# Kernel tuning notes

Hardware: AMD Instinct MI355X
Metric: run time of the kernel (lower is better)

The kernel has to match this reference:

```python
import jax, jax.numpy as jnp
import numpy as np

D_MODEL = 1024
N_HEADS = 16
D_HEAD = D_MODEL // N_HEADS
D_FF = 4096
BATCH = 2
SEQ = 2048
EPS = 1e-5


def setup_inputs() -> dict:
    key = jax.random.key(0)
    ks = jax.random.split(key, 8)
    s = 0.02
    x = jax.random.normal(ks[0], (BATCH, SEQ, D_MODEL), dtype=jnp.float32)
    # Per-head projection weights, stacked: [H, d_head, d_model] (torch Linear stores (out,in))
    wq = jax.random.normal(ks[1], (N_HEADS, D_HEAD, D_MODEL), dtype=jnp.float32) * s
    wk = jax.random.normal(ks[2], (N_HEADS, D_HEAD, D_MODEL), dtype=jnp.float32) * s
    wv = jax.random.normal(ks[3], (N_HEADS, D_HEAD, D_MODEL), dtype=jnp.float32) * s
    wo = jax.random.normal(ks[4], (D_MODEL, D_MODEL), dtype=jnp.float32) * s
    w1 = jax.random.normal(ks[5], (D_FF, D_MODEL), dtype=jnp.float32) * s
    w2 = jax.random.normal(ks[6], (D_MODEL, D_FF), dtype=jnp.float32) * s
    ln1_g = jnp.ones((D_MODEL,), jnp.float32)
    ln1_b = jnp.zeros((D_MODEL,), jnp.float32)
    ln2_g = jnp.ones((D_MODEL,), jnp.float32)
    ln2_b = jnp.zeros((D_MODEL,), jnp.float32)
    return {"x": x, "wq": wq, "wk": wk, "wv": wv, "wo": wo,
            "w1": w1, "w2": w2, "ln1_g": ln1_g, "ln1_b": ln1_b,
            "ln2_g": ln2_g, "ln2_b": ln2_b}


def _layer_norm(x, g, b):
    mu = jnp.mean(x, axis=-1, keepdims=True)
    var = jnp.mean(jnp.square(x - mu), axis=-1, keepdims=True)
    return (x - mu) * jax.lax.rsqrt(var + EPS) * g + b


def _mha(h, wq, wk, wv, wo):
    # h: [b,s,d]; wq/wk/wv: [H,dh,d] -> q/k/v: [b,H,s,dh]
    q = jnp.einsum('bsd,hed->bhse', h, wq)
    k = jnp.einsum('bsd,hed->bhse', h, wk)
    v = jnp.einsum('bsd,hed->bhse', h, wv)
    scores = jnp.einsum('bhqe,bhke->bhqk', q, k) / jnp.sqrt(jnp.float32(D_HEAD))
    weights = jax.nn.softmax(scores, axis=-1)
    ctx = jnp.einsum('bhqk,bhke->bhqe', weights, v)  # [b,H,s,dh]
    # concat heads in order (head 0 first) -> [b,s,H*dh]
    concat = jnp.transpose(ctx, (0, 2, 1, 3)).reshape(h.shape[0], h.shape[1], D_MODEL)
    return concat @ wo.T


def reference(x, wq, wk, wv, wo, w1, w2, ln1_g, ln1_b, ln2_g, ln2_b):
    h = _layer_norm(x, ln1_g, ln1_b)
    attn_out = _mha(h, wq, wk, wv, wo)
    h2 = _layer_norm(x + attn_out, ln2_g, ln2_b)
    ff = jax.nn.gelu(h2 @ w1.T, approximate=False) @ w2.T
    return x + ff
```

## Files before the change

kernel.cpp:

```cpp
#include <hip/hip_runtime.h>
#include <hip/hip_bf16.h>
#include <math.h>

typedef __bf16 bf16_t;
typedef __bf16 bf16x8 __attribute__((ext_vector_type(8)));
typedef __bf16 bf16x4 __attribute__((ext_vector_type(4)));
typedef float f32x4 __attribute__((ext_vector_type(4)));
typedef unsigned int u32;
typedef u32 u32x2 __attribute__((ext_vector_type(2)));

#define DM 1024
#define SEQL 2048
#define NTOK 4096
#define QKVN 3072

__device__ __forceinline__ void gload_lds16(const bf16_t* g, bf16_t* l){
  __builtin_amdgcn_global_load_lds((const __attribute__((address_space(1))) void*)g,
                                   (__attribute__((address_space(3))) void*)l, 16, 0, 0);
}
__device__ __forceinline__ u32 ldsoff(const void* p){
  return (u32)(size_t)(__attribute__((address_space(3))) const void*)p;
}
__device__ __forceinline__ u32x2 tr64(u32 byte_off){
  u32x2 d;
  asm volatile("ds_read_b64_tr_b16 %0, %1" : "=v"(d) : "v"(byte_off));
  return d;
}
__device__ __forceinline__ u32 pack2(float a, float b){
  union{ __bf16 h[2]; u32 w; } z;
  z.h[0]=(__bf16)a; z.h[1]=(__bf16)b; return z.w;
}
__device__ __forceinline__ float gelu_fast(float x){
  const float y = 0.79788456f*(x + 0.044715f*x*x*x);
  float a = y*2.885390082f;
  a = fminf(fmaxf(a, -30.f), 30.f);
  const float t = __builtin_amdgcn_exp2f(a);
  const float th = (t-1.0f)*__builtin_amdgcn_rcpf(t+1.0f);
  return 0.5f*x*(1.0f+th);
}

__global__ __launch_bounds__(256) void prep_kernel(
    const float* __restrict__ wq, const float* __restrict__ wk,
    const float* __restrict__ wv, const float* __restrict__ wo,
    const float* __restrict__ w1, const float* __restrict__ w2,
    const float* __restrict__ x,  const float* __restrict__ g1,
    const float* __restrict__ b1,
    bf16_t* __restrict__ wqkv_b, bf16_t* __restrict__ wo_b,
    bf16_t* __restrict__ w1_b,   bf16_t* __restrict__ w2_b,
    bf16_t* __restrict__ h1)
{
  __shared__ float red[8];
  const int bid = blockIdx.x;
  const int t = threadIdx.x;
  if (bid < 12288){
    const int flat = (bid*256 + t)*4;
    const int seg = flat >> 20;
    const int off1m = flat & 1048575;
    const float* src; bf16_t* dst;
    if (seg < 3){
      src = (seg==0 ? wq : (seg==1 ? wk : wv)) + off1m;
      dst = wqkv_b + flat;
    } else if (seg == 3){
      src = wo + off1m;  dst = wo_b + off1m;
    } else if (seg < 8){
      src = w1 + (flat - 4*1048576);  dst = w1_b + (flat - 4*1048576);
    } else {
      src = w2 + (flat - 8*1048576);  dst = w2_b + (flat - 8*1048576);
    }
    const float4 v = *(const float4*)src;
    bf16x4 o; o[0]=(__bf16)v.x; o[1]=(__bf16)v.y; o[2]=(__bf16)v.z; o[3]=(__bf16)v.w;
    *(bf16x4*)dst = o;
  } else {
    const int row = bid - 12288;
    const float4 v = *(const float4*)(x + (size_t)row*DM + t*4);
    float s  = v.x+v.y+v.z+v.w;
    float sq = v.x*v.x+v.y*v.y+v.z*v.z+v.w*v.w;
    #pragma unroll
    for (int m=1;m<64;m<<=1){ s += __shfl_xor(s,m); sq += __shfl_xor(sq,m); }
    const int w = t>>6;
    if ((t&63)==0){ red[w]=s; red[4+w]=sq; }
    __syncthreads();
    s  = red[0]+red[1]+red[2]+red[3];
    sq = red[4]+red[5]+red[6]+red[7];
    const float mean = s*(1.f/DM);
    const float var  = sq*(1.f/DM) - mean*mean;
    const float rstd = rsqrtf(var + 1e-5f);
    const float4 gg = *(const float4*)(g1 + t*4);
    const float4 bb = *(const float4*)(b1 + t*4);
    bf16x4 o;
    o[0]=(__bf16)((v.x-mean)*rstd*gg.x+bb.x);
    o[1]=(__bf16)((v.y-mean)*rstd*gg.y+bb.y);
    o[2]=(__bf16)((v.z-mean)*rstd*gg.z+bb.z);
    o[3]=(__bf16)((v.w-mean)*rstd*gg.w+bb.w);
    *(bf16x4*)(h1 + (size_t)row*DM + t*4) = o;
  }
}

__global__ __launch_bounds__(256) void lnb_kernel(const bf16_t* __restrict__ in,
    const float* __restrict__ g, const float* __restrict__ bta,
    bf16_t* __restrict__ outp)
{
  const int row = blockIdx.x;
  const int t = threadIdx.x;
  const bf16x4 raw = *(const bf16x4*)(in + (size_t)row*DM + t*4);
  float4 v;
  v.x=(float)raw[0]; v.y=(float)raw[1]; v.z=(float)raw[2]; v.w=(float)raw[3];
  float s  = v.x+v.y+v.z+v.w;
  float sq = v.x*v.x+v.y*v.y+v.z*v.z+v.w*v.w;
  #pragma unroll
  for (int m=1;m<64;m<<=1){ s += __shfl_xor(s,m); sq += __shfl_xor(sq,m); }
  __shared__ float red[8];
  const int w = t>>6;
  if ((t&63)==0){ red[w]=s; red[4+w]=sq; }
  __syncthreads();
  s  = red[0]+red[1]+red[2]+red[3];
  sq = red[4]+red[5]+red[6]+red[7];
  const float mean = s*(1.f/DM);
  const float var  = sq*(1.f/DM) - mean*mean;
  const float rstd = rsqrtf(var + 1e-5f);
  const float4 gg = *(const float4*)(g + t*4);
  const float4 bb = *(const float4*)(bta + t*4);
  bf16x4 o;
  o[0]=(__bf16)((v.x-mean)*rstd*gg.x+bb.x);
  o[1]=(__bf16)((v.y-mean)*rstd*gg.y+bb.y);
  o[2]=(__bf16)((v.z-mean)*rstd*gg.z+bb.z);
  o[3]=(__bf16)((v.w-mean)*rstd*gg.w+bb.w);
  *(bf16x4*)(outp + (size_t)row*DM + t*4) = o;
}

__global__ __launch_bounds__(256) void red4_kernel(
    const bf16_t* __restrict__ p0, const bf16_t* __restrict__ p1,
    const bf16_t* __restrict__ p2, const bf16_t* __restrict__ p3,
    const float* __restrict__ x, float* __restrict__ outp)
{
  const int i = (blockIdx.x*256 + threadIdx.x)*4;
  const bf16x4 a0 = *(const bf16x4*)(p0 + i);
  const bf16x4 a1 = *(const bf16x4*)(p1 + i);
  const bf16x4 a2 = *(const bf16x4*)(p2 + i);
  const bf16x4 a3 = *(const bf16x4*)(p3 + i);
  const float4 xs = *(const float4*)(x + i);
  float4 o;
  o.x = xs.x + ((float)a0[0]+(float)a1[0]) + ((float)a2[0]+(float)a3[0]);
  o.y = xs.y + ((float)a0[1]+(float)a1[1]) + ((float)a2[1]+(float)a3[1]);
  o.z = xs.z + ((float)a0[2]+(float)a1[2]) + ((float)a2[2]+(float)a3[2]);
  o.w = xs.w + ((float)a0[3]+(float)a1[3]) + ((float)a2[3]+(float)a3[3]);
  *(float4*)(outp + i) = o;
}

template<int EPI>
__global__ __launch_bounds__(512, 2) void gemm8ph(
    const bf16_t* __restrict__ A, const bf16_t* __restrict__ Bw,
    void* __restrict__ c0, void* __restrict__ c1,
    void* __restrict__ c2, void* __restrict__ c3,
    int N, int K, int lda)
{
  __shared__ __align__(16) char ldsb[131072];
  const int tid = threadIdx.x, lane = tid&63, wid = tid>>6;
  const int q16 = lane&15, g = lane>>4;
  const int wm = wid>>2, wn = wid&3;

  const int flat = blockIdx.y*gridDim.x + blockIdx.x;
  const int xcd = flat&7, jj = flat>>3;
  const int NY = gridDim.y;
  const int jdiv = jj/NY, jmod = jj - jdiv*NY;
  const int bm = (xcd*2 + jdiv)*256, bn = jmod*256;
  const int sk = blockIdx.z;
  const int koff = sk*K;
  void* Cout = (sk==0) ? c0 : (sk==1) ? c1 : (sk==2) ? c2 : c3;

  int mloc, kloc;
  {
    const u32 L = tid*16;
    const u32 logical = L ^ (((L>>9)&1)<<5);
    mloc = (int)(logical>>6);
    kloc = (int)((logical&63)>>1);
  }
  const bf16_t* asrc = A  + (size_t)(bm + mloc)*lda + koff + kloc;
  const bf16_t* bsrc = Bw + (size_t)(bn + mloc)*lda + koff + kloc;
  const u32 laneOff = ((u32)(q16*64 + g*16)) ^ ((u32)(q16&8)<<2);

  f32x4 acc[8][4] = {};
  bf16x8 bv[4];

  auto stage = [&](int buf, int kh, int isB, int s){
    const bf16_t* src = isB ? bsrc : asrc;
    #pragma unroll
    for (int h2=0; h2<2; h2++)
      gload_lds16(src + (size_t)(h2*128)*lda + s*64 + kh*32,
                  (bf16_t*)(ldsb + buf*65536 + isB*32768 + kh*16384 + h2*8192 + tid*16));
  };

  stage(0,0,0,0); stage(0,0,1,0); stage(0,1,0,0); stage(0,1,1,0);
  stage(1,0,0,1); stage(1,0,1,1);
  asm volatile("s_waitcnt vmcnt(4)" ::: "memory");
  __builtin_amdgcn_s_barrier();

  const int NSTEP = K>>6;
  const int NIT = NSTEP>>1;

#define PHASE(BUF,KH,MH,DOST,SBUF,SKH,SISB,SSTEP,CK) { \
    bf16x8 av[4]; \
    const char* Ab_ = ldsb + (BUF)*65536 + (KH)*16384 + wm*8192; \
    _Pragma("unroll") for (int jx=0;jx<4;jx++) \
      av[jx] = *(const bf16x8*)(Ab_ + (((MH)*4+jx)<<10) + laneOff); \
    if ((MH)==0){ \
      const char* Bb_ = ldsb + (BUF)*65536 + 32768 + (KH)*16384 + (wn>>1)*8192; \
      _Pragma("unroll") for (int jx=0;jx<4;jx++) \
        bv[jx] = *(const bf16x8*)(Bb_ + ((((wn&1)*4)+jx)<<10) + laneOff); \
    } \
    if (DOST) stage(SBUF,SKH,SISB,SSTEP); \
    asm volatile("s_barrier" ::: "memory"); \
    asm volatile("s_waitcnt lgkmcnt(0)" ::: "memory"); \
    __builtin_amdgcn_s_setprio(1); \
    _Pragma("unroll") for (int jx=0;jx<4;jx++) \
      _Pragma("unroll") for (int j2=0;j2<4;j2++) \
        acc[(MH)*4+jx][j2] = __builtin_amdgcn_mfma_f32_16x16x32_bf16(av[jx], bv[j2], acc[(MH)*4+jx][j2],0,0,0); \
    __builtin_amdgcn_s_setprio(0); \
    if (CK){ if (nl) { asm volatile("s_waitcnt vmcnt(4)" ::: "memory"); } \
             else    { asm volatile("s_waitcnt vmcnt(0)" ::: "memory"); } } \
    asm volatile("s_barrier" ::: "memory"); }

  for (int it=0; it<NIT; it++){
    const int s0 = 2*it, s1 = s0+1;
    const bool nl = (it+1 < NIT);
    PHASE(0,0,0, 1,  1,1,0, s1,   0)
    PHASE(0,0,1, 1,  1,1,1, s1,   0)
    PHASE(0,1,0, nl, 0,0,0, s0+2, 0)
    PHASE(0,1,1, nl, 0,0,1, s0+2, 1)
    PHASE(1,0,0, nl, 0,1,0, s0+2, 0)
    PHASE(1,0,1, nl, 0,1,1, s0+2, 0)
    PHASE(1,1,0, nl, 1,0,0, s1+2, 0)
    PHASE(1,1,1, nl, 1,0,1, s1+2, 1)
  }
#undef PHASE

  #pragma unroll
  for (int fm=0; fm<8; fm++)
    #pragma unroll
    for (int fn=0; fn<4; fn++)
      #pragma unroll
      for (int i=0; i<4; i++){
        const int r = bm + wm*128 + fm*16 + g*4 + i;
        const int c = bn + wn*64 + fn*16 + q16;
        const size_t idx = (size_t)r*N + c;
        const float vv = acc[fm][fn][i];
        if constexpr (EPI==0){
          ((bf16_t*)Cout)[idx] = (__bf16)vv;
        } else {
          ((bf16_t*)Cout)[idx] = (__bf16)gelu_fast(vv);
        }
      }
}

template<int EPI>
__global__ __launch_bounds__(512, 2) void gemm128(
    const bf16_t* __restrict__ A, const bf16_t* __restrict__ Bw,
    void* __restrict__ Cout, const float* __restrict__ X,
    int N, int K)
{
  constexpr int BK = 32;
  __shared__ __align__(16) char ldsb[3*16384];
  const int tid = threadIdx.x, lane = tid&63, wid = tid>>6;
  const int q16 = lane&15, g = lane>>4;
  const int wm = wid>>2, wn = wid&3;

  const int flat = blockIdx.y*gridDim.x + blockIdx.x;
  const int xcd = flat&7, j = flat>>3;
  const int bm = ((xcd<<2) + (j>>3))*128, bn = (j&7)*128;

  int mloc, kloc;
  {
    const u32 L = tid*16;
    const u32 logical = L ^ (((L>>9)&1)<<5);
    mloc = (int)(logical>>6);
    kloc = (int)((logical&63)>>1);
  }
  const bf16_t* asrc = A  + (size_t)(bm + mloc)*K + kloc;
  const bf16_t* bsrc = Bw + (size_t)(bn + mloc)*K + kloc;
  const u32 laneOff = ((u32)(q16*64 + g*16)) ^ ((u32)(q16&8)<<2);

  f32x4 acc[4][2] = {};

  auto stageA = [&](int buf, int k0){
    gload_lds16(asrc + k0, (bf16_t*)(ldsb + buf*16384 + tid*16));
  };
  auto stageB = [&](int buf, int k0){
    gload_lds16(bsrc + k0, (bf16_t*)(ldsb + buf*16384 + 8192 + tid*16));
  };

  stageA(0,0); stageB(0,0);
  stageA(1,BK); stageB(1,BK);
  asm volatile("s_waitcnt vmcnt(2)" ::: "memory");
  __builtin_amdgcn_s_barrier();

  const int NT = K/BK;
  int bcur = 0;
  for (int kt=0; kt<NT; kt++){
    const int bstg = (bcur >= 1) ? bcur-1 : bcur+2;
    const char* Ab = ldsb + bcur*16384 + wm*4096;
    const char* Bb = ldsb + bcur*16384 + 8192 + wn*2048;
    const bool sOK = (kt+2 < NT);
    const int k0s = (kt+2)*BK;
    bf16x8 bv[2];
    #pragma unroll
    for (int p=0; p<2; p++){
      bf16x8 av[2];
      #pragma unroll
      for (int jx=0;jx<2;jx++)
        av[jx] = *(const bf16x8*)(Ab + ((p*2+jx)<<10) + laneOff);
      if (p==0){
        #pragma unroll
        for (int jx=0;jx<2;jx++)
          bv[jx] = *(const bf16x8*)(Bb + (jx<<10) + laneOff);
      }
      if (sOK){
        if (p==0) stageA(bstg,k0s);
        else      stageB(bstg,k0s);
      }
      asm volatile("s_barrier" ::: "memory");
      __builtin_amdgcn_s_setprio(1);
      #pragma unroll
      for (int jx=0;jx<2;jx++)
        #pragma unroll
        for (int j2=0;j2<2;j2++)
          acc[p*2+jx][j2] = __builtin_amdgcn_mfma_f32_16x16x32_bf16(av[jx], bv[j2], acc[p*2+jx][j2], 0,0,0);
      __builtin_amdgcn_s_setprio(0);
      if (p==1){
        if (sOK) asm volatile("s_waitcnt vmcnt(2)" ::: "memory");
        else     asm volatile("s_waitcnt vmcnt(0)" ::: "memory");
      }
      asm volatile("s_barrier" ::: "memory");
    }
    bcur = (bcur==2)?0:bcur+1;
  }

  #pragma unroll
  for (int fm=0; fm<4; fm++)
    #pragma unroll
    for (int fn=0; fn<2; fn++)
      #pragma unroll
      for (int i=0; i<4; i++){
        const int r = bm + wm*64 + fm*16 + g*4 + i;
        const int c = bn + wn*32 + fn*16 + q16;
        const size_t idx = (size_t)r*N + c;
        const float vv = X[idx] + acc[fm][fn][i];
        ((bf16_t*)Cout)[idx] = (__bf16)vv;
      }
}

__global__ __launch_bounds__(512, 4) void attn_kernel(
    const bf16_t* __restrict__ QKV, bf16_t* __restrict__ Ctx)
{
  __shared__ __align__(16) bf16_t Ks[2][128*64];
  __shared__ __align__(16) bf16_t Vs[2][32*4*72];
  const int tid = threadIdx.x, lane = tid&63, w = tid>>6;
  const int g = lane>>4, q16 = lane&15;
  const int bh = blockIdx.y, b = bh>>4, h = bh&15;
  const int qr0 = blockIdx.x*128 + w*16;
  const size_t tok0 = (size_t)b*SEQL;
  const int ch0 = h*64;

  bf16x8 aq[2];
  #pragma unroll
  for (int ks=0; ks<2; ks++){
    bf16x8 t = *(const bf16x8*)(QKV + (tok0+qr0+q16)*QKVN + ch0 + ks*32 + g*8);
    #pragma unroll
    for (int jx=0;jx<8;jx++) t[jx] = (__bf16)((float)t[jx]*0.18033688f);
    aq[ks] = t;
  }

  const int srow = tid>>3, sc8 = (tid&7)*8;
  const bf16_t* kptr_swz = QKV + (tok0+srow)*QKVN + 1024 + ch0 + (sc8 ^ ((srow&7)<<3));
  const bf16_t* vptr = QKV + (tok0+srow)*QKVN + 2048 + ch0 + sc8;
  const int vwoff = ((srow>>2)*4 + (sc8>>4))*72 + (srow&3)*16 + (sc8&15);

  float mrun = -1e30f, lrun = 0.f;
  f32x4 o[4] = {};

  #pragma unroll
  for (int it=0; it<2; it++)
    gload_lds16(kptr_swz + (size_t)(it*64)*QKVN, &Ks[0][tid*8 + it*4096]);
  bf16x8 vreg[2];
  #pragma unroll
  for (int it=0; it<2; it++)
    vreg[it] = *(const bf16x8*)(vptr + (size_t)(it*64)*QKVN);
  #pragma unroll
  for (int it=0; it<2; it++)
    *(bf16x8*)&Vs[0][vwoff + it*4608] = vreg[it];
  #pragma unroll
  for (int it=0; it<2; it++)
    vreg[it] = *(const bf16x8*)(vptr + (size_t)(128 + it*64)*QKVN);

  const int NT = SEQL/128;
  for (int t=0; t<NT; t++){
    __syncthreads();
    if (t+1 < NT){
      #pragma unroll
      for (int it=0; it<2; it++){
        gload_lds16(kptr_swz + (size_t)((t+1)*128 + it*64)*QKVN, &Ks[(t+1)&1][tid*8 + it*4096]);
        *(bf16x8*)&Vs[(t+1)&1][vwoff + it*4608] = vreg[it];
      }
      if (t+2 < NT){
        #pragma unroll
        for (int it=0; it<2; it++)
          vreg[it] = *(const bf16x8*)(vptr + (size_t)((t+2)*128 + it*64)*QKVN);
      }
    }
    const bf16_t* ksb = Ks[t&1];
    const u32 vs0 = ldsoff(&Vs[t&1][0]);

    f32x4 s[8] = {};
    #pragma unroll
    for (int ks=0; ks<2; ks++){
      #pragma unroll
      for (int fn=0; fn<8; fn++){
        const int r = fn*16 + q16;
        const int ce = ks*32 + g*8;
        bf16x8 bk = *(const bf16x8*)&ksb[r*64 + (ce ^ ((r&7)<<3))];
        s[fn] = __builtin_amdgcn_mfma_f32_16x16x32_bf16(bk, aq[ks], s[fn], 0, 0, 0);
      }
    }

    float mx = -1e30f;
    #pragma unroll
    for (int fn=0; fn<8; fn++)
      mx = fmaxf(mx, fmaxf(fmaxf(s[fn][0],s[fn][1]), fmaxf(s[fn][2],s[fn][3])));
    mx = fmaxf(mx, __shfl_xor(mx,16));
    mx = fmaxf(mx, __shfl_xor(mx,32));

    if (!__all(mx <= mrun + 11.54f)){
      const float mnew = fmaxf(mrun, mx);
      const float alpha = __builtin_amdgcn_exp2f(mrun - mnew);
      #pragma unroll
      for (int i=0;i<4;i++){
        const float ai = __shfl(alpha, g*4+i);
        o[0][i]*=ai; o[1][i]*=ai; o[2][i]*=ai; o[3][i]*=ai;
      }
      lrun *= alpha;
      mrun = mnew;
    }

    float rs = 0.f;
    u32 u[8][2];
    #pragma unroll
    for (int fn=0; fn<8; fn++){
      const float e0=__builtin_amdgcn_exp2f(s[fn][0]-mrun);
      const float e1=__builtin_amdgcn_exp2f(s[fn][1]-mrun);
      const float e2=__builtin_amdgcn_exp2f(s[fn][2]-mrun);
      const float e3=__builtin_amdgcn_exp2f(s[fn][3]-mrun);
      rs += (e0+e1)+(e2+e3);
      u[fn][0] = pack2(e0,e1);
      u[fn][1] = pack2(e2,e3);
    }
    rs += __shfl_xor(rs,16);
    rs += __shfl_xor(rs,32);
    lrun += rs;

    {
      u32x2 loA[4], hiA[4], loB[4], hiB[4];
      #pragma unroll
      for (int ne=0; ne<4; ne++){
        const u32 vb = vs0 + (u32)(((2*g*4 + ne)*72 + q16)*2);
        loA[ne] = tr64(vb);
        hiA[ne] = tr64(vb + 576);
      }
      #pragma unroll
      for (int ks=0; ks<4; ks++){
        union { u32 wd[4]; bf16x8 v; } pa;
        #pragma unroll
        for (int jj=0; jj<4; jj++){
          const int src = q16 + ((((g&1)<<1) + (jj>>1))<<4);
          const u32 a0 = (u32)__shfl((int)u[2*ks  ][jj&1], src);
          const u32 a1 = (u32)__shfl((int)u[2*ks+1][jj&1], src);
          pa.wd[jj] = (g&2) ? a1 : a0;
        }
        if (ks < 3){
          u32x2* nl_ = (ks&1) ? loA : loB;
          u32x2* nh_ = (ks&1) ? hiA : hiB;
          #pragma unroll
          for (int ne=0; ne<4; ne++){
            const u32 vb = vs0 + (u32)(((((ks+1)*8 + 2*g)*4 + ne)*72 + q16)*2);
            nl_[ne] = tr64(vb);
            nh_[ne] = tr64(vb + 576);
          }
          asm volatile("s_waitcnt lgkmcnt(8)" ::: "memory");
        } else {
          asm volatile("s_waitcnt lgkmcnt(0)" ::: "memory");
        }
        __builtin_amdgcn_sched_barrier(0);
        const u32x2* lo = (ks&1) ? loB : loA;
        const u32x2* hi = (ks&1) ? hiB : hiA;
        union { u32x2 u2[2]; bf16x8 v; } cc;
        #pragma unroll
        for (int ne=0; ne<4; ne++){
          cc.u2[0]=lo[ne]; cc.u2[1]=hi[ne];
          o[ne] = __builtin_amdgcn_mfma_f32_16x16x32_bf16(pa.v, cc.v, o[ne], 0, 0, 0);
        }
      }
    }
  }

  const float rl = 1.0f/lrun;
  #pragma unroll
  for (int i=0; i<4; i++){
    const float ri = __shfl(rl, g*4+i);
    #pragma unroll
    for (int ne=0; ne<4; ne++){
      const int r = qr0 + g*4 + i;
      Ctx[(tok0+r)*DM + ch0 + ne*16 + q16] = (__bf16)(o[ne][i]*ri);
    }
  }
}

extern "C" void kernel_launch(void* const* d_in, const int* in_sizes, int n_in,
                              void* d_out, int out_size, void* d_ws, size_t ws_size,
                              hipStream_t stream)
{
  (void)in_sizes; (void)n_in; (void)out_size; (void)ws_size;
  const float* x  = (const float*)d_in[0];
  const float* wq = (const float*)d_in[1];
  const float* wk = (const float*)d_in[2];
  const float* wv = (const float*)d_in[3];
  const float* wo = (const float*)d_in[4];
  const float* w1 = (const float*)d_in[5];
  const float* w2 = (const float*)d_in[6];
  const float* g1 = (const float*)d_in[7];
  const float* b1 = (const float*)d_in[8];
  const float* g2 = (const float*)d_in[9];
  const float* b2 = (const float*)d_in[10];
  float* out = (float*)d_out;
  char* ws = (char*)d_ws;
  const size_t MB = 1024ull*1024ull;

  bf16_t* wqkv_b = (bf16_t*)(ws);
  bf16_t* wo_b   = (bf16_t*)(ws + 6*MB);
  bf16_t* w1_b   = (bf16_t*)(ws + 8*MB);
  bf16_t* w2_b   = (bf16_t*)(ws + 16*MB);
  bf16_t* h1     = (bf16_t*)(ws + 24*MB);
  bf16_t* qkv    = (bf16_t*)(ws + 32*MB);
  bf16_t* ctx    = (bf16_t*)(ws + 56*MB);
  bf16_t* res2b  = (bf16_t*)(ws + 64*MB);
  bf16_t* h2     = h1;
  bf16_t* ffm    = (bf16_t*)(ws + 32*MB);
  bf16_t* p0     = (bf16_t*)(ws);
  bf16_t* p1     = (bf16_t*)(ws + 8*MB);
  bf16_t* p2     = (bf16_t*)(ws + 24*MB);
  bf16_t* p3     = (bf16_t*)(ws + 64*MB);

  prep_kernel<<<16384, 256, 0, stream>>>(wq, wk, wv, wo, w1, w2, x, g1, b1,
                                         wqkv_b, wo_b, w1_b, w2_b, h1);
  gemm8ph<0><<<dim3(16, 12), 512, 0, stream>>>(h1, wqkv_b, (void*)qkv, (void*)qkv,
                                               (void*)qkv, (void*)qkv, QKVN, 1024, 1024);
  attn_kernel<<<dim3(16, 32), 512, 0, stream>>>(qkv, ctx);
  gemm128<0><<<dim3(32, 8), 512, 0, stream>>>(ctx, wo_b, (void*)res2b, x, 1024, 1024);
  lnb_kernel<<<NTOK, 256, 0, stream>>>(res2b, g2, b2, h2);
  gemm8ph<2><<<dim3(16, 16), 512, 0, stream>>>(h2, w1_b, (void*)ffm, (void*)ffm,
                                               (void*)ffm, (void*)ffm, 4096, 1024, 1024);
  gemm8ph<0><<<dim3(16, 4, 4), 512, 0, stream>>>(ffm, w2_b, (void*)p0, (void*)p1,
                                                 (void*)p2, (void*)p3, 1024, 1024, 4096);
  red4_kernel<<<4096, 256, 0, stream>>>(p0, p1, p2, p3, x, out);
}
```

Measured before the change: 233.0 us.

## Raise wave priority around attention MFMAs and widen red4 loads

Wraps the QK^T and PV MFMA loops in the attention kernel with s_setprio so matrix waves get issue priority over softmax and load waves. It also restructures the row-max reduction into a chained form and makes the final split-K reduction kernel process eight elements per thread with 16-byte bf16 loads, halving its grid. The gain hinges on how scheduling priority interacts with the other waves on the CU, and the max-chain change may lengthen the dependency chain.

```diff
diff --git a/kernel.cpp b/kernel.cpp
--- a/kernel.cpp
+++ b/kernel.cpp
@@ -133,18 +133,21 @@
     const bf16_t* __restrict__ p2, const bf16_t* __restrict__ p3,
     const float* __restrict__ x, float* __restrict__ outp)
 {
-  const int i = (blockIdx.x*256 + threadIdx.x)*4;
-  const bf16x4 a0 = *(const bf16x4*)(p0 + i);
-  const bf16x4 a1 = *(const bf16x4*)(p1 + i);
-  const bf16x4 a2 = *(const bf16x4*)(p2 + i);
-  const bf16x4 a3 = *(const bf16x4*)(p3 + i);
-  const float4 xs = *(const float4*)(x + i);
-  float4 o;
-  o.x = xs.x + ((float)a0[0]+(float)a1[0]) + ((float)a2[0]+(float)a3[0]);
-  o.y = xs.y + ((float)a0[1]+(float)a1[1]) + ((float)a2[1]+(float)a3[1]);
-  o.z = xs.z + ((float)a0[2]+(float)a1[2]) + ((float)a2[2]+(float)a3[2]);
-  o.w = xs.w + ((float)a0[3]+(float)a1[3]) + ((float)a2[3]+(float)a3[3]);
-  *(float4*)(outp + i) = o;
+  const int i = (blockIdx.x*256 + threadIdx.x)*8;
+  const bf16x8 a0 = *(const bf16x8*)(p0 + i);
+  const bf16x8 a1 = *(const bf16x8*)(p1 + i);
+  const bf16x8 a2 = *(const bf16x8*)(p2 + i);
+  const bf16x8 a3 = *(const bf16x8*)(p3 + i);
+  #pragma unroll
+  for (int h=0; h<2; h++){
+    const float4 xs = *(const float4*)(x + i + h*4);
+    float4 o;
+    o.x = xs.x + ((float)a0[h*4+0]+(float)a1[h*4+0]) + ((float)a2[h*4+0]+(float)a3[h*4+0]);
+    o.y = xs.y + ((float)a0[h*4+1]+(float)a1[h*4+1]) + ((float)a2[h*4+1]+(float)a3[h*4+1]);
+    o.z = xs.z + ((float)a0[h*4+2]+(float)a1[h*4+2]) + ((float)a2[h*4+2]+(float)a3[h*4+2]);
+    o.w = xs.w + ((float)a0[h*4+3]+(float)a1[h*4+3]) + ((float)a2[h*4+3]+(float)a3[h*4+3]);
+    *(float4*)(outp + i + h*4) = o;
+  }
 }
 
 template<int EPI>
@@ -410,6 +413,7 @@
     const u32 vs0 = ldsoff(&Vs[t&1][0]);
 
     f32x4 s[8] = {};
+    __builtin_amdgcn_s_setprio(1);
     #pragma unroll
     for (int ks=0; ks<2; ks++){
       #pragma unroll
@@ -420,11 +424,14 @@
         s[fn] = __builtin_amdgcn_mfma_f32_16x16x32_bf16(bk, aq[ks], s[fn], 0, 0, 0);
       }
     }
+    __builtin_amdgcn_s_setprio(0);
 
     float mx = -1e30f;
     #pragma unroll
-    for (int fn=0; fn<8; fn++)
-      mx = fmaxf(mx, fmaxf(fmaxf(s[fn][0],s[fn][1]), fmaxf(s[fn][2],s[fn][3])));
+    for (int fn=0; fn<8; fn++){
+      const float a = fmaxf(fmaxf(s[fn][0], s[fn][1]), s[fn][2]);
+      mx = fmaxf(fmaxf(mx, a), s[fn][3]);
+    }
     mx = fmaxf(mx, __shfl_xor(mx,16));
     mx = fmaxf(mx, __shfl_xor(mx,32));
 
@@ -491,11 +498,13 @@
         const u32x2* lo = (ks&1) ? loB : loA;
         const u32x2* hi = (ks&1) ? hiB : hiA;
         union { u32x2 u2[2]; bf16x8 v; } cc;
+        __builtin_amdgcn_s_setprio(1);
         #pragma unroll
         for (int ne=0; ne<4; ne++){
           cc.u2[0]=lo[ne]; cc.u2[1]=hi[ne];
           o[ne] = __builtin_amdgcn_mfma_f32_16x16x32_bf16(pa.v, cc.v, o[ne], 0, 0, 0);
         }
+        __builtin_amdgcn_s_setprio(0);
       }
     }
   }
@@ -558,5 +567,5 @@
                                                (void*)ffm, (void*)ffm, 4096, 1024, 1024);
   gemm8ph<0><<<dim3(16, 4, 4), 512, 0, stream>>>(ffm, w2_b, (void*)p0, (void*)p1,
                                                  (void*)p2, (void*)p3, 1024, 1024, 4096);
-  red4_kernel<<<4096, 256, 0, stream>>>(p0, p1, p2, p3, x, out);
-}
+  red4_kernel<<<2048, 256, 0, stream>>>(p0, p1, p2, p3, x, out);
+}
```

Measured after the change: 232.4 us (median of 2 runs). About the same (-0.3%).
